# Optimization experiments

Hardware: AMD Instinct MI355X
Metric: run time of the kernel (lower is better)

Reference implementation:

```python
import jax, jax.numpy as jnp
import numpy as np

QMAX = 7.0            # int4 narrow range: [-7, 7]
SCALING_MIN_VAL = 2e-16


def fake_quant_weight_per_channel(w):
    """Brevitas CommonIntWeightPerChannelQuant, bit_width=4.

    Per-output-channel float scale from abs-max stats, narrow-range signed
    int4 round+clamp, then dequantize. STE so gradients pass through.
    w: [O, I, KH, KW]
    """
    amax = jnp.max(jnp.abs(w), axis=(1, 2, 3), keepdims=True)   # [O,1,1,1]
    scale = jnp.maximum(amax / QMAX, SCALING_MIN_VAL)
    wq = jnp.clip(jnp.round(w / scale), -QMAX, QMAX) * scale
    # straight-through estimator (matches Brevitas round_ste backward)
    return w + jax.lax.stop_gradient(wq - w)


def setup_inputs() -> dict:
    key = jax.random.key(0)
    kx, kw = jax.random.split(key)
    x = jax.random.normal(kx, (32, 256, 56, 56), dtype=jnp.float32)
    # conv weight [out_channels, in_channels, kh, kw]
    w = jax.random.normal(kw, (256, 256, 3, 3), dtype=jnp.float32) * 0.05
    return {"x": x, "w": w}


def reference(x, w):
    wq = fake_quant_weight_per_channel(w)
    return jax.lax.conv_general_dilated(
        x, wq,
        window_strides=(1, 1),
        padding=((1, 1), (1, 1)),
        dimension_numbers=("NCHW", "OIHW", "NCHW"),
    )
```

## Files before the change

kernel.cpp:

```cpp
#include <hip/hip_runtime.h>
#include <cstdint>
#include <cstddef>

typedef __bf16 bf16x8 __attribute__((ext_vector_type(8)));
typedef float  f32x4  __attribute__((ext_vector_type(4)));
typedef float  f32x16 __attribute__((ext_vector_type(16)));
typedef int    i32x4  __attribute__((ext_vector_type(4)));

#define QMAX 7.0f
#define SCALE_MIN 2e-16f

#define BAR()    asm volatile("s_barrier" ::: "memory")
#define WAITV0() asm volatile("s_waitcnt vmcnt(0)" ::: "memory")

__global__ __launch_bounds__(256) void quant_w_kernel(const float* __restrict__ w,
                                                      __bf16* __restrict__ wq) {
    const int o = blockIdx.x;
    const int t = threadIdx.x;
    const float* wo = w + (size_t)o * 2304;

    float vals[9];
    float m = 0.f;
    #pragma unroll
    for (int i = 0; i < 9; ++i) {
        float v = wo[t + i * 256];
        vals[i] = v;
        m = fmaxf(m, fabsf(v));
    }
    #pragma unroll
    for (int off = 32; off >= 1; off >>= 1) m = fmaxf(m, __shfl_down(m, off));
    __shared__ float red[4];
    __shared__ float s_scale;
    if ((t & 63) == 0) red[t >> 6] = m;
    __syncthreads();
    if (t == 0) {
        float am = fmaxf(fmaxf(red[0], red[1]), fmaxf(red[2], red[3]));
        s_scale = fmaxf(am / QMAX, SCALE_MIN);
    }
    __syncthreads();
    const float scale = s_scale;

    #pragma unroll
    for (int i = 0; i < 9; ++i) {
        int idx = t + i * 256;
        int c = idx / 9;
        int tap = idx - c * 9;
        float q = rintf(vals[i] / scale);
        q = fminf(QMAX, fmaxf(-QMAX, q));
        wq[(size_t)tap * 65536 + (size_t)o * 256 + c] = (__bf16)(q * scale);
    }
}

__global__ __launch_bounds__(256) void convert_x_kernel(const float* __restrict__ x,
                                                        __bf16* __restrict__ xpad) {
    __shared__ float tile[32][33];
    const int n  = blockIdx.z;
    const int c0 = blockIdx.y * 32;
    const int p0 = blockIdx.x * 32;
    const int tx = threadIdx.x & 31;
    const int ty = threadIdx.x >> 5;

    #pragma unroll
    for (int r = 0; r < 4; ++r) {
        int c = c0 + ty + r * 8;
        tile[ty + r * 8][tx] = x[((size_t)(n * 256 + c)) * 3136 + p0 + tx];
    }
    __syncthreads();
    #pragma unroll
    for (int r = 0; r < 4; ++r) {
        int p = p0 + ty + r * 8;
        int h = p / 56, wcol = p - h * 56;
        xpad[(((size_t)n * 58 + h + 1) * 58 + (wcol + 1)) * 256 + c0 + tx] =
            (__bf16)tile[tx][ty + r * 8];
    }
}

__global__ __launch_bounds__(256) void zero_halo_kernel(__bf16* __restrict__ xpad) {
    const int t = blockIdx.x * 256 + threadIdx.x;
    const int cvec = t & 31;
    const int r    = t >> 5;
    const int n    = r / 228;
    const int pos  = r - n * 228;
    if (n >= 32) return;
    int h, wcol;
    if      (pos < 58)  { h = 0;          wcol = pos; }
    else if (pos < 116) { h = 57;         wcol = pos - 58; }
    else if (pos < 172) { h = pos - 115;  wcol = 0; }
    else                { h = pos - 171;  wcol = 57; }
    i32x4* dst = (i32x4*)(xpad + (((size_t)n * 58 + h) * 58 + wcol) * 256);
    dst[cvec] = (i32x4){0, 0, 0, 0};
}

__device__ __forceinline__ void gload_lds16(const void* g, void* l) {
    __builtin_amdgcn_global_load_lds((const __attribute__((address_space(1))) void*)g,
                                     (__attribute__((address_space(3))) void*)l,
                                     16, 0, 0);
}

__global__ __launch_bounds__(512, 2) void conv_mfma_kernel(const __bf16* __restrict__ xpad,
                                                           const __bf16* __restrict__ wq,
                                                           float* __restrict__ out) {
    extern __shared__ __align__(16) char lds[];
    const int tid  = threadIdx.x;
    const int wv   = tid >> 6;
    const int lane = tid & 63;
    const int bid  = blockIdx.x;
    const int swz  = (bid & 7) * 49 + (bid >> 3);
    const int p0   = swz * 256;

    const int wr = wv >> 2;
    const int wc = wv & 3;

    const int srow  = wv * 8 + (lane >> 3);
    const int schunk = (lane & 7) ^ (lane >> 3);
    const __bf16* pAg = wq + (size_t)srow * 256 + schunk * 8;
    const __bf16* pB[4];
    #pragma unroll
    for (int p = 0; p < 4; ++p) {
        int pos = p0 + p * 64 + srow;
        int ni = pos / 3136;
        int hw = pos - ni * 3136;
        int h = hw / 56, w = hw - h * 56;
        pB[p] = xpad + (((size_t)ni * 58 + h) * 58 + w) * 256 + schunk * 8;
    }

    const int hi = lane >> 5;
    int kxo[4];
    #pragma unroll
    for (int ks = 0; ks < 4; ++ks)
        kxo[ks] = ((ks * 2 + hi) ^ (lane & 7)) * 16;
    const int arowb = (wr * 128 + (lane & 31)) * 128;
    const int browb = (wc * 64  + (lane & 31)) * 128;

    f32x16 acc[4][2];
    #pragma unroll
    for (int m = 0; m < 4; ++m)
        #pragma unroll
        for (int n = 0; n < 2; ++n)
            acc[m][n] = (f32x16)(0.f);

    {
        char* wa = lds;
        char* wb = lds + 32768;
        #pragma unroll
        for (int p = 0; p < 4; ++p) {
            gload_lds16(pAg + p * 16384, wa + (p * 64 + wv * 8) * 128);
            gload_lds16(pB[p],           wb + (p * 64 + wv * 8) * 128);
        }
        WAITV0();
        BAR();
    }

    for (int s = 0; s < 36; ++s) {
        const int cur = s & 1;
        const char* Ard = lds + (cur ? 65536 : 0);
        const char* Brd = Ard + 32768;
        char* Awr = lds + (cur ? 0 : 65536);
        char* Bwr = Awr + 32768;
        const bool stg = (s < 35);
        int aoffN = 0, boffN = 0;
        if (stg) {
            const int sn = s + 1;
            const int tapN = sn >> 2, ccN = sn & 3;
            const int khN = tapN / 3, kwN = tapN - khN * 3;
            aoffN = tapN * 65536 + ccN * 64;
            boffN = (khN * 58 + kwN) * 256 + ccN * 64;
        }

        bf16x8 a0[4], a1[4], b0[4], b1[4];

        if (stg) {
            gload_lds16(pAg + 0 * 16384 + aoffN, Awr + (0 * 64 + wv * 8) * 128);
            gload_lds16(pB[0] + boffN,           Bwr + (0 * 64 + wv * 8) * 128);
        }
        #pragma unroll
        for (int ks = 0; ks < 4; ++ks) {
            a0[ks] = *(const bf16x8*)(Ard + arowb + 0 * 4096 + kxo[ks]);
            a1[ks] = *(const bf16x8*)(Ard + arowb + 1 * 4096 + kxo[ks]);
            b0[ks] = *(const bf16x8*)(Brd + browb + 0 * 4096 + kxo[ks]);
        }
        BAR();
        __builtin_amdgcn_s_setprio(1);
        #pragma unroll
        for (int ks = 0; ks < 4; ++ks) {
            acc[0][0] = __builtin_amdgcn_mfma_f32_32x32x16_bf16(a0[ks], b0[ks], acc[0][0], 0, 0, 0);
            acc[1][0] = __builtin_amdgcn_mfma_f32_32x32x16_bf16(a1[ks], b0[ks], acc[1][0], 0, 0, 0);
        }
        __builtin_amdgcn_s_setprio(0);
        BAR();

        if (stg) {
            gload_lds16(pAg + 1 * 16384 + aoffN, Awr + (1 * 64 + wv * 8) * 128);
            gload_lds16(pB[1] + boffN,           Bwr + (1 * 64 + wv * 8) * 128);
        }
        #pragma unroll
        for (int ks = 0; ks < 4; ++ks)
            b1[ks] = *(const bf16x8*)(Brd + browb + 1 * 4096 + kxo[ks]);
        BAR();
        __builtin_amdgcn_s_setprio(1);
        #pragma unroll
        for (int ks = 0; ks < 4; ++ks) {
            acc[0][1] = __builtin_amdgcn_mfma_f32_32x32x16_bf16(a0[ks], b1[ks], acc[0][1], 0, 0, 0);
            acc[1][1] = __builtin_amdgcn_mfma_f32_32x32x16_bf16(a1[ks], b1[ks], acc[1][1], 0, 0, 0);
        }
        __builtin_amdgcn_s_setprio(0);
        BAR();

        if (stg) {
            gload_lds16(pAg + 2 * 16384 + aoffN, Awr + (2 * 64 + wv * 8) * 128);
            gload_lds16(pB[2] + boffN,           Bwr + (2 * 64 + wv * 8) * 128);
        }
        #pragma unroll
        for (int ks = 0; ks < 4; ++ks) {
            a0[ks] = *(const bf16x8*)(Ard + arowb + 2 * 4096 + kxo[ks]);
            a1[ks] = *(const bf16x8*)(Ard + arowb + 3 * 4096 + kxo[ks]);
        }
        BAR();
        __builtin_amdgcn_s_setprio(1);
        #pragma unroll
        for (int ks = 0; ks < 4; ++ks) {
            acc[2][0] = __builtin_amdgcn_mfma_f32_32x32x16_bf16(a0[ks], b0[ks], acc[2][0], 0, 0, 0);
            acc[3][0] = __builtin_amdgcn_mfma_f32_32x32x16_bf16(a1[ks], b0[ks], acc[3][0], 0, 0, 0);
        }
        __builtin_amdgcn_s_setprio(0);
        BAR();

        if (stg) {
            gload_lds16(pAg + 3 * 16384 + aoffN, Awr + (3 * 64 + wv * 8) * 128);
            gload_lds16(pB[3] + boffN,           Bwr + (3 * 64 + wv * 8) * 128);
        }
        BAR();
        __builtin_amdgcn_s_setprio(1);
        #pragma unroll
        for (int ks = 0; ks < 4; ++ks) {
            acc[2][1] = __builtin_amdgcn_mfma_f32_32x32x16_bf16(a0[ks], b1[ks], acc[2][1], 0, 0, 0);
            acc[3][1] = __builtin_amdgcn_mfma_f32_32x32x16_bf16(a1[ks], b1[ks], acc[3][1], 0, 0, 0);
        }
        __builtin_amdgcn_s_setprio(0);
        BAR();

        WAITV0();
        BAR();
    }

    #pragma unroll
    for (int n = 0; n < 2; ++n) {
        const int pos = p0 + wc * 64 + n * 32 + (lane & 31);
        const int ni = pos / 3136;
        const int hw = pos - ni * 3136;
        float* ob = out + (size_t)ni * 802816 + hw;
        #pragma unroll
        for (int m = 0; m < 4; ++m) {
            const int om = wr * 128 + m * 32 + 4 * hi;
            #pragma unroll
            for (int r = 0; r < 16; ++r) {
                const int o = om + (r & 3) + 8 * (r >> 2);
                ob[(size_t)o * 3136] = acc[m][n][r];
            }
        }
    }
}

__global__ __launch_bounds__(256) void conv_naive_kernel(const float* __restrict__ x,
                                                         const float* __restrict__ w,
                                                         float* __restrict__ out) {
    const int n = blockIdx.z;
    const int o = blockIdx.y;
    const int strip = blockIdx.x;
    __shared__ float wqs[2304];
    __shared__ float red[4];
    __shared__ float s_scale;
    const float* wo = w + (size_t)o * 2304;
    float m = 0.f;
    for (int i = threadIdx.x; i < 2304; i += 256) m = fmaxf(m, fabsf(wo[i]));
    #pragma unroll
    for (int off = 32; off >= 1; off >>= 1) m = fmaxf(m, __shfl_down(m, off));
    if ((threadIdx.x & 63) == 0) red[threadIdx.x >> 6] = m;
    __syncthreads();
    if (threadIdx.x == 0) {
        float am = fmaxf(fmaxf(red[0], red[1]), fmaxf(red[2], red[3]));
        s_scale = fmaxf(am / QMAX, SCALE_MIN);
    }
    __syncthreads();
    const float scale = s_scale;
    for (int i = threadIdx.x; i < 2304; i += 256) {
        float q = rintf(wo[i] / scale);
        q = fminf(QMAX, fmaxf(-QMAX, q));
        wqs[i] = q * scale;
    }
    __syncthreads();
    int p = strip * 256 + threadIdx.x;
    if (p >= 3136) return;
    int h = p / 56, wcol = p - h * 56;
    float acc = 0.f;
    for (int c = 0; c < 256; ++c) {
        const float* xc = x + ((size_t)(n * 256 + c)) * 3136;
        const float* wk = wqs + c * 9;
        #pragma unroll
        for (int kh = 0; kh < 3; ++kh) {
            int hh = h + kh - 1;
            if (hh < 0 || hh > 55) continue;
            #pragma unroll
            for (int kw = 0; kw < 3; ++kw) {
                int ww2 = wcol + kw - 1;
                if (ww2 < 0 || ww2 > 55) continue;
                acc += xc[hh * 56 + ww2] * wk[kh * 3 + kw];
            }
        }
    }
    out[((size_t)(n * 256 + o)) * 3136 + p] = acc;
}

extern "C" void kernel_launch(void* const* d_in, const int* in_sizes, int n_in,
                              void* d_out, int out_size, void* d_ws, size_t ws_size,
                              hipStream_t stream) {
    const float* x = (const float*)d_in[0];
    const float* w = (const float*)d_in[1];
    float* out = (float*)d_out;

    const size_t WQ_BYTES   = 9ull * 256 * 256 * 2;
    const size_t XPAD_OFF   = WQ_BYTES;
    const size_t XPAD_BYTES = 32ull * 58 * 58 * 256 * 2;

    if (ws_size >= XPAD_OFF + XPAD_BYTES) {
        __bf16* wq   = (__bf16*)d_ws;
        __bf16* xpad = (__bf16*)((char*)d_ws + XPAD_OFF);
        hipFuncSetAttribute((const void*)conv_mfma_kernel,
                            hipFuncAttributeMaxDynamicSharedMemorySize, 131072);
        zero_halo_kernel<<<912, 256, 0, stream>>>(xpad);
        quant_w_kernel<<<256, 256, 0, stream>>>(w, wq);
        convert_x_kernel<<<dim3(98, 8, 32), 256, 0, stream>>>(x, xpad);
        conv_mfma_kernel<<<392, 512, 131072, stream>>>(xpad, wq, out);
    } else {
        conv_naive_kernel<<<dim3(13, 256, 32), 256, 0, stream>>>(x, w, out);
    }
}
```

Baseline: 185.5 us.

## Replace full vmcnt drain with fine-grained waits and reorder staged loads

Reassigns global-to-LDS staging so each wave loads rows grouped to match the order in which the consumers read A and B sub-tiles. The end-of-iteration vmcnt(0) drain is replaced by partial vmcnt waits before each LDS read phase, so loads for the next stage stay in flight across the iteration boundary. Several barriers are also removed. This is meant to hide global load latency behind the MFMA work. The risk is correctness, since the vmcnt counts must exactly match the load issue order across waves.

```diff
diff --git a/kernel.cpp b/kernel.cpp
--- a/kernel.cpp
+++ b/kernel.cpp
@@ -10,8 +10,8 @@
 #define QMAX 7.0f
 #define SCALE_MIN 2e-16f
 
-#define BAR()    asm volatile("s_barrier" ::: "memory")
-#define WAITV0() asm volatile("s_waitcnt vmcnt(0)" ::: "memory")
+#define BAR()     asm volatile("s_barrier" ::: "memory")
+#define WAITVM(N) asm volatile("s_waitcnt vmcnt(" #N ")" ::: "memory")
 
 __global__ __launch_bounds__(256) void quant_w_kernel(const float* __restrict__ w,
                                                       __bf16* __restrict__ wq) {
@@ -111,18 +111,21 @@
     const int wr = wv >> 2;
     const int wc = wv & 3;
 
-    const int srow  = wv * 8 + (lane >> 3);
     const int schunk = (lane & 7) ^ (lane >> 3);
-    const __bf16* pAg = wq + (size_t)srow * 256 + schunk * 8;
+    const int srowA = (wv >> 2) * 128 + (wv & 3) * 8 + (lane >> 3);
+    const __bf16* pAg = wq + (size_t)srowA * 256 + schunk * 8;
+    const int srowB = (wv >> 1) * 64 + (wv & 1) * 8 + (lane >> 3);
     const __bf16* pB[4];
     #pragma unroll
-    for (int p = 0; p < 4; ++p) {
-        int pos = p0 + p * 64 + srow;
+    for (int j = 0; j < 4; ++j) {
+        int pos = p0 + srowB + j * 16;
         int ni = pos / 3136;
         int hw = pos - ni * 3136;
         int h = hw / 56, w = hw - h * 56;
-        pB[p] = xpad + (((size_t)ni * 58 + h) * 58 + w) * 256 + schunk * 8;
-    }
+        pB[j] = xpad + (((size_t)ni * 58 + h) * 58 + w) * 256 + schunk * 8;
+    }
+    const int adst = ((wv >> 2) * 128 + (wv & 3) * 8) * 128;
+    const int bdst = ((wv >> 1) * 64  + (wv & 1) * 8) * 128;
 
     const int hi = lane >> 5;
     int kxo[4];
@@ -140,15 +143,16 @@
             acc[m][n] = (f32x16)(0.f);
 
     {
-        char* wa = lds;
-        char* wb = lds + 32768;
-        #pragma unroll
-        for (int p = 0; p < 4; ++p) {
-            gload_lds16(pAg + p * 16384, wa + (p * 64 + wv * 8) * 128);
-            gload_lds16(pB[p],           wb + (p * 64 + wv * 8) * 128);
-        }
-        WAITV0();
-        BAR();
+        char* Aw = lds;
+        char* Bw = lds + 32768;
+        gload_lds16(pAg + 0 * 8192, Aw + adst + 0 * 4096);
+        gload_lds16(pB[0],          Bw + bdst + 0 * 2048);
+        gload_lds16(pAg + 1 * 8192, Aw + adst + 1 * 4096);
+        gload_lds16(pB[1],          Bw + bdst + 1 * 2048);
+        gload_lds16(pB[2],          Bw + bdst + 2 * 2048);
+        gload_lds16(pB[3],          Bw + bdst + 3 * 2048);
+        gload_lds16(pAg + 2 * 8192, Aw + adst + 2 * 4096);
+        gload_lds16(pAg + 3 * 8192, Aw + adst + 3 * 4096);
     }
 
     for (int s = 0; s < 36; ++s) {
@@ -158,28 +162,31 @@
         char* Awr = lds + (cur ? 0 : 65536);
         char* Bwr = Awr + 32768;
         const bool stg = (s < 35);
-        int aoffN = 0, boffN = 0;
+        size_t aoffN = 0, boffN = 0;
         if (stg) {
             const int sn = s + 1;
             const int tapN = sn >> 2, ccN = sn & 3;
             const int khN = tapN / 3, kwN = tapN - khN * 3;
-            aoffN = tapN * 65536 + ccN * 64;
-            boffN = (khN * 58 + kwN) * 256 + ccN * 64;
+            aoffN = (size_t)tapN * 65536 + ccN * 64;
+            boffN = (size_t)(khN * 58 + kwN) * 256 + ccN * 64;
         }
 
         bf16x8 a0[4], a1[4], b0[4], b1[4];
 
-        if (stg) {
-            gload_lds16(pAg + 0 * 16384 + aoffN, Awr + (0 * 64 + wv * 8) * 128);
-            gload_lds16(pB[0] + boffN,           Bwr + (0 * 64 + wv * 8) * 128);
-        }
+        WAITVM(4);
+        BAR();
         #pragma unroll
         for (int ks = 0; ks < 4; ++ks) {
             a0[ks] = *(const bf16x8*)(Ard + arowb + 0 * 4096 + kxo[ks]);
             a1[ks] = *(const bf16x8*)(Ard + arowb + 1 * 4096 + kxo[ks]);
             b0[ks] = *(const bf16x8*)(Brd + browb + 0 * 4096 + kxo[ks]);
         }
-        BAR();
+        if (stg) {
+            gload_lds16(pAg + 0 * 8192 + aoffN, Awr + adst + 0 * 4096);
+            gload_lds16(pB[0] + boffN,          Bwr + bdst + 0 * 2048);
+            gload_lds16(pAg + 1 * 8192 + aoffN, Awr + adst + 1 * 4096);
+            gload_lds16(pB[1] + boffN,          Bwr + bdst + 1 * 2048);
+        }
         __builtin_amdgcn_s_setprio(1);
         #pragma unroll
         for (int ks = 0; ks < 4; ++ks) {
@@ -189,14 +196,15 @@
         __builtin_amdgcn_s_setprio(0);
         BAR();
 
-        if (stg) {
-            gload_lds16(pAg + 1 * 16384 + aoffN, Awr + (1 * 64 + wv * 8) * 128);
-            gload_lds16(pB[1] + boffN,           Bwr + (1 * 64 + wv * 8) * 128);
-        }
+        if (stg) { WAITVM(6); } else { WAITVM(2); }
+        BAR();
         #pragma unroll
         for (int ks = 0; ks < 4; ++ks)
             b1[ks] = *(const bf16x8*)(Brd + browb + 1 * 4096 + kxo[ks]);
-        BAR();
+        if (stg) {
+            gload_lds16(pB[2] + boffN, Bwr + bdst + 2 * 2048);
+            gload_lds16(pB[3] + boffN, Bwr + bdst + 3 * 2048);
+        }
         __builtin_amdgcn_s_setprio(1);
         #pragma unroll
         for (int ks = 0; ks < 4; ++ks) {
@@ -206,16 +214,17 @@
         __builtin_amdgcn_s_setprio(0);
         BAR();
 
-        if (stg) {
-            gload_lds16(pAg + 2 * 16384 + aoffN, Awr + (2 * 64 + wv * 8) * 128);
-            gload_lds16(pB[2] + boffN,           Bwr + (2 * 64 + wv * 8) * 128);
-        }
+        if (stg) { WAITVM(6); } else { WAITVM(0); }
+        BAR();
         #pragma unroll
         for (int ks = 0; ks < 4; ++ks) {
             a0[ks] = *(const bf16x8*)(Ard + arowb + 2 * 4096 + kxo[ks]);
             a1[ks] = *(const bf16x8*)(Ard + arowb + 3 * 4096 + kxo[ks]);
         }
-        BAR();
+        if (stg) {
+            gload_lds16(pAg + 2 * 8192 + aoffN, Awr + adst + 2 * 4096);
+            gload_lds16(pAg + 3 * 8192 + aoffN, Awr + adst + 3 * 4096);
+        }
         __builtin_amdgcn_s_setprio(1);
         #pragma unroll
         for (int ks = 0; ks < 4; ++ks) {
@@ -225,11 +234,6 @@
         __builtin_amdgcn_s_setprio(0);
         BAR();
 
-        if (stg) {
-            gload_lds16(pAg + 3 * 16384 + aoffN, Awr + (3 * 64 + wv * 8) * 128);
-            gload_lds16(pB[3] + boffN,           Bwr + (3 * 64 + wv * 8) * 128);
-        }
-        BAR();
         __builtin_amdgcn_s_setprio(1);
         #pragma unroll
         for (int ks = 0; ks < 4; ++ks) {
@@ -237,9 +241,6 @@
             acc[3][1] = __builtin_amdgcn_mfma_f32_32x32x16_bf16(a1[ks], b1[ks], acc[3][1], 0, 0, 0);
         }
         __builtin_amdgcn_s_setprio(0);
-        BAR();
-
-        WAITV0();
         BAR();
     }
 
```

Result: faster. 173.2 us (-6.6%).
